# Kernel tuning notes

Measured on AMD Instinct MI355X. Metric: run time of the kernel, lower is better.

The kernel has to match this reference:

```python
import jax, jax.numpy as jnp
import numpy as np

B, T, P = 4, 512, 3584          # batch, new tokens per seq, cached tokens per seq
D_MODEL, H, KH, DH = 2048, 16, 4, 128
N_REP = H // KH
MAX_SEQ = 4096
ROPE_BASE = 1e6
EPS = 1e-6


def _rmsnorm(t, w):
    # t: [..., DH]
    var = jnp.mean(t * t, axis=-1, keepdims=True)
    return t * jax.lax.rsqrt(var + EPS) * w


def _rope(t, positions):
    # t: [N, heads, DH], positions: [N] int
    half = DH // 2
    inv_freq = (1.0 / ROPE_BASE) ** (2.0 * jnp.arange(half, dtype=jnp.float32) / DH)
    theta = positions.astype(jnp.float32)[:, None] * inv_freq[None, :]   # [N, half]
    theta = jnp.concatenate([theta, theta], axis=-1)                      # [N, DH]
    sin = jnp.sin(theta)[:, None, :]
    cos = jnp.cos(theta)[:, None, :]
    x1, x2 = jnp.split(t, 2, axis=-1)
    rot = jnp.concatenate([-x2, x1], axis=-1)
    return cos * t + sin * rot


def setup_inputs() -> dict:
    key = jax.random.key(0)
    ks = jax.random.split(key, 9)
    N = B * T
    x = jax.random.normal(ks[0], (N, D_MODEL), dtype=jnp.float32)
    k_cache = jax.random.normal(ks[1], (B, KH, P, DH), dtype=jnp.float32)
    v_cache = jax.random.normal(ks[2], (B, KH, P, DH), dtype=jnp.float32)
    s = 1.0 / np.sqrt(D_MODEL)
    w_q = jax.random.normal(ks[3], (H * DH, D_MODEL), dtype=jnp.float32) * s
    w_k = jax.random.normal(ks[4], (KH * DH, D_MODEL), dtype=jnp.float32) * s
    w_v = jax.random.normal(ks[5], (KH * DH, D_MODEL), dtype=jnp.float32) * s
    w_o = jax.random.normal(ks[6], (D_MODEL, H * DH), dtype=jnp.float32) * s
    q_norm_w = jnp.ones((DH,), dtype=jnp.float32)
    k_norm_w = jnp.ones((DH,), dtype=jnp.float32)
    # each sequence's new tokens occupy absolute positions [P, P+T)
    positions = jnp.tile(P + jnp.arange(T, dtype=jnp.int32), B)  # [B*T]
    return {"x": x, "k_cache": k_cache, "v_cache": v_cache,
            "w_q": w_q, "w_k": w_k, "w_v": w_v, "w_o": w_o,
            "q_norm_w": q_norm_w, "k_norm_w": k_norm_w,
            "positions": positions}


def reference(x, k_cache, v_cache, w_q, w_k, w_v, w_o, q_norm_w, k_norm_w, positions):
    N = x.shape[0]
    # QKV projections (no bias)
    q = (x @ w_q.T).reshape(N, H, DH)
    k = (x @ w_k.T).reshape(N, KH, DH)
    v = (x @ w_v.T).reshape(N, KH, DH)
    # per-head RMSNorm then RoPE at absolute positions
    q = _rope(_rmsnorm(q, q_norm_w), positions)
    k = _rope(_rmsnorm(k, k_norm_w), positions)
    # assemble full KV: cached (pre-rotated) past + new tokens
    k_new = k.reshape(B, T, KH, DH).transpose(0, 2, 1, 3)   # [B,KH,T,DH]
    v_new = v.reshape(B, T, KH, DH).transpose(0, 2, 1, 3)
    k_full = jnp.concatenate([k_cache, k_new], axis=2)       # [B,KH,P+T,DH]
    v_full = jnp.concatenate([v_cache, v_new], axis=2)
    # GQA: repeat each kv head n_rep times
    k_rep = jnp.repeat(k_full, N_REP, axis=1)                # [B,H,S,DH]
    v_rep = jnp.repeat(v_full, N_REP, axis=1)
    q4 = q.reshape(B, T, H, DH).transpose(0, 2, 1, 3)        # [B,H,T,DH]
    scale = 1.0 / jnp.sqrt(jnp.float32(DH))
    scores = jnp.einsum('bhtd,bhsd->bhts', q4, k_rep) * scale  # [B,H,T,P+T]
    # right-bottom causal mask: q_pos = P + t, kv_pos = s
    q_pos = P + jnp.arange(T)
    kv_pos = jnp.arange(P + T)
    mask = q_pos[:, None] >= kv_pos[None, :]
    scores = jnp.where(mask[None, None], scores, -jnp.inf)
    attn = jax.nn.softmax(scores, axis=-1)
    out = jnp.einsum('bhts,bhsd->bhtd', attn, v_rep)          # [B,H,T,DH]
    out = out.transpose(0, 2, 1, 3).reshape(N, H * DH)
    return out @ w_o.T
```

## Files before the change

### kernel.cpp

```cpp
#include <hip/hip_runtime.h>
#include <hip/hip_bf16.h>
#include <stdint.h>

#define B_   4
#define T_   512
#define P_   3584
#define S_   4096
#define H_   16
#define KH_  4
#define DM_  2048
#define DH_  128
#define NTOK 2048
#define NCHUNK 3
#define NROWS 32768

typedef __attribute__((ext_vector_type(8)))  short          bf16x8;
typedef __attribute__((ext_vector_type(4)))  float          f32x4;
typedef __attribute__((ext_vector_type(16))) float          f32x16;
typedef __attribute__((ext_vector_type(4)))  float          f4v;
typedef __attribute__((ext_vector_type(4)))  unsigned short us4v;

__device__ __forceinline__ unsigned short f2bf(float x) {
    union { float f; unsigned u; } v; v.f = x;
    unsigned r = v.u + 0x7FFFu + ((v.u >> 16) & 1u);
    return (unsigned short)(r >> 16);
}
__device__ __forceinline__ float bf2f(unsigned short b) {
    union { unsigned u; float f; } v; v.u = ((unsigned)b) << 16; return v.f;
}
__device__ __forceinline__ unsigned pkbf(float a, float b) {
    __hip_bfloat162 h = __float22bfloat162_rn(float2{a, b});
    union { __hip_bfloat162 h; unsigned u; } cv; cv.h = h; return cv.u;
}
__device__ __forceinline__ float ex2(float x) {
    float r; asm("v_exp_f32 %0, %1" : "=v"(r) : "v"(x)); return r;
}
__device__ __forceinline__ float max3f(float a, float b, float c) {
    float r; asm("v_max3_f32 %0, %1, %2, %3" : "=v"(r) : "v"(a), "v"(b), "v"(c)); return r;
}
__device__ __forceinline__ float sin_rev(float xf) {
    float r; asm("v_sin_f32 %0, %1" : "=v"(r) : "v"(xf)); return r;
}
__device__ __forceinline__ float cos_rev(float xf) {
    float r; asm("v_cos_f32 %0, %1" : "=v"(r) : "v"(xf)); return r;
}

#define GLDS16(gp, lp) __builtin_amdgcn_global_load_lds( \
    (const __attribute__((address_space(1))) void*)(gp), \
    (__attribute__((address_space(3))) void*)(lp), 16, 0, 0)

__global__ __launch_bounds__(256) void convert_all(
    const float* __restrict__ x,  const float* __restrict__ wq,
    const float* __restrict__ wk, const float* __restrict__ wv,
    const float* __restrict__ wo, const float* __restrict__ kc,
    unsigned short* __restrict__ xb,   unsigned short* __restrict__ wqkvb,
    unsigned short* __restrict__ wob,  unsigned short* __restrict__ kfull)
{
    const long total = 5505024;
    for (long i = (long)blockIdx.x * 256 + threadIdx.x; i < total;
         i += (long)gridDim.x * 256) {
        const f4v* src; us4v* dst; long s4, d4;
        if (i < 1048576)      { src=(const f4v*)x;  dst=(us4v*)xb;              s4=i;         d4=s4; }
        else if (i < 2097152) { src=(const f4v*)wq; dst=(us4v*)wqkvb;           s4=i-1048576; d4=s4; }
        else if (i < 2359296) { src=(const f4v*)wk; dst=(us4v*)(wqkvb+4194304); s4=i-2097152; d4=s4; }
        else if (i < 2621440) { src=(const f4v*)wv; dst=(us4v*)(wqkvb+5242880); s4=i-2359296; d4=s4; }
        else if (i < 3670016) { src=(const f4v*)wo; dst=(us4v*)wob;             s4=i-2621440; d4=s4; }
        else                  { s4=i-3670016; long bk=s4/114688;
                                d4=bk*131072+(s4-bk*114688);
                                src=(const f4v*)kc; dst=(us4v*)kfull; }
        f4v v = src[s4];
        us4v o; o[0]=f2bf(v[0]); o[1]=f2bf(v[1]); o[2]=f2bf(v[2]); o[3]=f2bf(v[3]);
        dst[d4] = o;
    }
}

__global__ __launch_bounds__(256) void vcache_transpose(
    const float* __restrict__ vc, unsigned short* __restrict__ vT)
{
    __shared__ unsigned short tile[64][65];
    const int bk = blockIdx.z;
    const int st = blockIdx.x;
    const int dt = blockIdx.y;
    const float* src = vc + ((size_t)bk * P_ + st * 64) * DH_ + dt * 64;
    const int tq = threadIdx.x & 15;
    const int ts = threadIdx.x >> 4;
    #pragma unroll
    for (int i = 0; i < 4; ++i) {
        const int si = ts + i * 16;
        f4v v = *(const f4v*)(src + (size_t)si * DH_ + tq * 4);
        tile[si][tq*4+0] = f2bf(v[0]); tile[si][tq*4+1] = f2bf(v[1]);
        tile[si][tq*4+2] = f2bf(v[2]); tile[si][tq*4+3] = f2bf(v[3]);
    }
    __syncthreads();
    unsigned short* dst = vT + ((size_t)bk * DH_ + dt * 64) * S_ + st * 64;
    const int sq = threadIdx.x & 15;
    const int td = threadIdx.x >> 4;
    #pragma unroll
    for (int i = 0; i < 4; ++i) {
        const int di = td + i * 16;
        us4v o;
        o[0] = tile[sq*4+0][di]; o[1] = tile[sq*4+1][di];
        o[2] = tile[sq*4+2][di]; o[3] = tile[sq*4+3][di];
        *(us4v*)(dst + (size_t)di * S_ + sq * 4) = o;
    }
}

__global__ __launch_bounds__(256) void gemm_bt(
    const unsigned short* __restrict__ A, const unsigned short* __restrict__ Bw,
    void* __restrict__ C, int M, int N, int K, int obf16)
{
    __shared__ short As[2][128 * 32];
    __shared__ short Bs[2][128 * 32];
    const int tid = threadIdx.x, lane = tid & 63, w = tid >> 6;
    const int nbn = N >> 7;
    const int bm = blockIdx.x / nbn, bn = blockIdx.x % nbn;
    const int m0 = bm << 7, n0 = bn << 7;
    const int wm = w >> 1, wn = w & 1;

    f32x4 acc[4][4];
    #pragma unroll
    for (int i = 0; i < 4; ++i)
        #pragma unroll
        for (int j = 0; j < 4; ++j)
            #pragma unroll
            for (int r = 0; r < 4; ++r) acc[i][j][r] = 0.f;

    const int arow = lane >> 2;
    const int acol = (lane & 3) << 3;

    auto stage = [&](int buf, int k0) {
        #pragma unroll
        for (int cc = 0; cc < 2; ++cc) {
            const int c = 2 * w + cc;
            GLDS16(A  + (size_t)(m0 + c * 16 + arow) * K + k0 + acol, &As[buf][c * 512]);
            GLDS16(Bw + (size_t)(n0 + c * 16 + arow) * K + k0 + acol, &Bs[buf][c * 512]);
        }
    };

    stage(0, 0);
    __syncthreads();

    const int nk = K >> 5;
    const int fr = lane & 15, fk = (lane >> 4) << 3;
    for (int t = 0; t < nk; ++t) {
        const int buf = t & 1;
        if (t + 1 < nk) stage(buf ^ 1, (t + 1) << 5);
        bf16x8 a[4], b[4];
        #pragma unroll
        for (int i = 0; i < 4; ++i)
            a[i] = *(const bf16x8*)&As[buf][(wm * 64 + i * 16 + fr) * 32 + fk];
        #pragma unroll
        for (int j = 0; j < 4; ++j)
            b[j] = *(const bf16x8*)&Bs[buf][(wn * 64 + j * 16 + fr) * 32 + fk];
        #pragma unroll
        for (int i = 0; i < 4; ++i)
            #pragma unroll
            for (int j = 0; j < 4; ++j)
                acc[i][j] = __builtin_amdgcn_mfma_f32_16x16x32_bf16(a[i], b[j], acc[i][j], 0, 0, 0);
        __syncthreads();
    }

    const int er = lane >> 4, ec = lane & 15;
    #pragma unroll
    for (int i = 0; i < 4; ++i)
        #pragma unroll
        for (int j = 0; j < 4; ++j)
            #pragma unroll
            for (int r = 0; r < 4; ++r) {
                const int row = m0 + wm * 64 + i * 16 + er * 4 + r;
                const int col = n0 + wn * 64 + j * 16 + ec;
                if (obf16) ((unsigned short*)C)[(size_t)row * N + col] = f2bf(acc[i][j][r]);
                else       ((float*)C)[(size_t)row * N + col] = acc[i][j][r];
            }
}

__global__ __launch_bounds__(256) void norm_rope(
    const unsigned short* __restrict__ qkv, const float* __restrict__ qw,
    const float* __restrict__ kw,  const int* __restrict__ pos,
    unsigned short* __restrict__ Qb, unsigned short* __restrict__ Kf,
    unsigned short* __restrict__ VT)
{
    const int task = blockIdx.x * 4 + (threadIdx.x >> 6);
    const int n = task / 24, idx = task % 24;
    const int lane = threadIdx.x & 63;
    const int b = n >> 9, t = n & 511;

    if (idx >= 20) {
        const int kh = idx - 20;
        const unsigned short* src = qkv + (size_t)n * 3072 + 2560 + kh * 128;
        unsigned short* dstT = VT + (size_t)(b * KH_ + kh) * DH_ * S_ + (P_ + t);
        dstT[(size_t)lane * S_]        = src[lane];
        dstT[(size_t)(lane + 64) * S_] = src[lane + 64];
        return;
    }
    const bool isq = idx < 16;
    const int hh = isq ? idx : (idx - 16);
    const unsigned short* src = qkv + (size_t)n * 3072 + (isq ? hh * 128 : 2048 + hh * 128);
    const float* wn_ = isq ? qw : kw;
    float x0 = bf2f(src[lane]), x1 = bf2f(src[lane + 64]);
    float ss = x0 * x0 + x1 * x1;
    #pragma unroll
    for (int m = 1; m < 64; m <<= 1) ss += __shfl_xor(ss, m);
    const float rinv = rsqrtf(ss * (1.0f / 128.0f) + 1e-6f);
    float y0 = x0 * rinv * wn_[lane];
    float y1 = x1 * rinv * wn_[lane + 64];
    const float fr = ex2(-(float)lane * (19.931568569324174f / 64.0f));
    const float th = (float)pos[n] * fr;
    const float xr = th * 0.15915494309189535f;
    const float xf = xr - floorf(xr);
    const float sn = sin_rev(xf), cs = cos_rev(xf);
    float o0 = cs * y0 - sn * y1;
    float o1 = cs * y1 + sn * y0;
    unsigned short* dst;
    if (isq) {
        const float qs = 0.08838834764831845f * 1.4426950408889634f;
        o0 *= qs; o1 *= qs;
        dst = Qb + ((size_t)(b * H_ + hh) * T_ + t) * DH_;
    } else {
        dst = Kf + ((size_t)(b * KH_ + hh) * S_ + P_ + t) * DH_;
    }
    dst[lane]      = f2bf(o0);
    dst[lane + 64] = f2bf(o1);
}

__global__ __launch_bounds__(256, 3) void attn(
    const unsigned short* __restrict__ Qb, const unsigned short* __restrict__ Kf,
    const unsigned short* __restrict__ VT, unsigned short* __restrict__ op0,
    unsigned short* __restrict__ op1, unsigned short* __restrict__ op2,
    float2* __restrict__ ml)
{
    __shared__ short Ks[3][32 * 128];
    __shared__ short Vs[3][128 * 32];

    const int tid = threadIdx.x, lane = tid & 63, w = tid >> 6;
    const int c = blockIdx.x >> 8;
    const int y = blockIdx.x & 255;
    const int xcd = y & 7, slot = y >> 3;
    const int p = xcd + 8 * (slot >> 4);
    const int inner = slot & 15;
    const int b = p >> 2, kvh = p & 3;
    const int h = kvh * 4 + (inner >> 2);
    const int qt = inner & 3;
    const int t0 = qt * 128;

    const unsigned short* Qrow = Qb + (size_t)(b * H_ + h) * T_ * DH_;
    const unsigned short* Kb   = Kf + (size_t)(b * KH_ + kvh) * S_ * DH_;
    const unsigned short* VTb  = VT + (size_t)(b * KH_ + kvh) * DH_ * S_;

    const int ql = lane & 31;
    const int hi = lane >> 5;

    bf16x8 qf[8];
    {
        const unsigned short* qp = Qrow + (size_t)(t0 + w * 32 + ql) * DH_ + hi * 8;
        #pragma unroll
        for (int d0 = 0; d0 < 8; ++d0) qf[d0] = *(const bf16x8*)(qp + d0 * 16);
    }

    f32x16 o[4];
    #pragma unroll
    for (int d = 0; d < 4; ++d)
        #pragma unroll
        for (int r = 0; r < 16; ++r) o[d][r] = 0.f;
    float m_run = -INFINITY, l_run = 0.f;

    const int q_pos = P_ + t0 + w * 32 + ql;
    const int s_end_wave = P_ + t0 + w * 32 + 32;
    const int nt_full = (P_ + t0 + 128) >> 5;
    const int nj = (nt_full - c + 2) / 3;

    auto stage = [&](int buf, int tile) {
        const int s0 = tile << 5;
        #pragma unroll
        for (int cc = 0; cc < 2; ++cc) {
            const int cx = 2 * w + cc;
            const int krow = cx * 4 + (lane >> 4);
            const int kel  = 8 * ((lane & 15) ^ (krow & 15));
            GLDS16(Kb + (size_t)(s0 + krow) * DH_ + kel, &Ks[buf][cx * 512]);
            const int vrow = cx * 16 + (lane >> 2);
            const int vel  = 8 * ((lane & 3) ^ ((lane >> 3) & 3));
            GLDS16(VTb + (size_t)vrow * S_ + s0 + vel, &Vs[buf][cx * 512]);
        }
    };

    stage(0, c);
    if (nj > 1) stage(1, c + 3);

    for (int j = 0; j < nj; ++j) {
        if (j + 1 < nj) asm volatile("s_waitcnt vmcnt(4)" ::: "memory");
        else            asm volatile("s_waitcnt vmcnt(0)" ::: "memory");
        __builtin_amdgcn_s_barrier();
        if (j + 2 < nj) stage((j + 2) % 3, c + 3 * (j + 2));

        const int t = c + 3 * j;
        const int s0 = t << 5;
        const int buf = j % 3;
        if (s0 < s_end_wave) {
            f32x16 st;
            #pragma unroll
            for (int r = 0; r < 16; ++r) st[r] = 0.f;
            {
                const char* kbase = (const char*)&Ks[buf][0] + ql * 256;
                const int sw = 16 * (ql & 15);
                #pragma unroll
                for (int d0 = 0; d0 < 8; ++d0) {
                    bf16x8 kfr = *(const bf16x8*)(kbase + ((d0 * 32 + 16 * hi) ^ sw));
                    st = __builtin_amdgcn_mfma_f32_32x32x16_bf16(kfr, qf[d0], st, 0, 0, 0);
                }
            }
            if (s0 + 31 > P_ + t0 + w * 32) {
                #pragma unroll
                for (int r = 0; r < 16; ++r) {
                    const int srow = (r & 3) + 8 * (r >> 2) + 4 * hi;
                    if (s0 + srow > q_pos) st[r] = -INFINITY;
                }
            }
            float m0_ = max3f(st[0], st[1], st[2]),  m1_ = max3f(st[3], st[4], st[5]);
            float m2_ = max3f(st[6], st[7], st[8]),  m3_ = max3f(st[9], st[10], st[11]);
            float m4_ = max3f(st[12], st[13], st[14]);
            float pmax = fmaxf(max3f(m0_, m1_, m2_), max3f(m3_, m4_, st[15]));
            pmax = fmaxf(pmax, __shfl_xor(pmax, 32));
            if (!__all(pmax <= m_run + 11.5f)) {
                const float m_new = fmaxf(m_run, pmax);
                const float alpha = ex2(m_run - m_new);
                l_run *= alpha;
                #pragma unroll
                for (int r = 0; r < 16; ++r) {
                    const int qr = (r & 3) + 8 * (r >> 2) + 4 * hi;
                    const float a = __shfl(alpha, qr);
                    #pragma unroll
                    for (int d = 0; d < 4; ++d) o[d][r] *= a;
                }
                m_run = m_new;
            }
            float pv[16]; float psum = 0.f;
            #pragma unroll
            for (int r = 0; r < 16; ++r) { pv[r] = ex2(st[r] - m_run); psum += pv[r]; }
            psum += __shfl_xor(psum, 32);
            l_run += psum;
            unsigned pk[8];
            #pragma unroll
            for (int u = 0; u < 8; ++u) pk[u] = pkbf(pv[2 * u], pv[2 * u + 1]);
            unsigned xw[8];
            #pragma unroll
            for (int u = 0; u < 8; ++u) xw[u] = (unsigned)__shfl_xor((int)pk[u], 32);
            union { bf16x8 v; unsigned u[4]; } pa0, pa1;
            pa0.u[0] = hi ? xw[2] : pk[0];  pa0.u[1] = hi ? xw[3] : pk[1];
            pa0.u[2] = hi ? pk[2] : xw[0];  pa0.u[3] = hi ? pk[3] : xw[1];
            pa1.u[0] = hi ? xw[6] : pk[4];  pa1.u[1] = hi ? xw[7] : pk[5];
            pa1.u[2] = hi ? pk[6] : xw[4];  pa1.u[3] = hi ? pk[7] : xw[5];
            #pragma unroll
            for (int ch = 0; ch < 2; ++ch)
                #pragma unroll
                for (int db = 0; db < 4; ++db) {
                    const int vrow = db * 32 + ql;
                    bf16x8 vf = *(const bf16x8*)&Vs[buf][vrow * 32 + 8 * ((2 * ch + hi) ^ ((ql >> 1) & 3))];
                    o[db] = __builtin_amdgcn_mfma_f32_32x32x16_bf16(
                        ch ? pa1.v : pa0.v, vf, o[db], 0, 0, 0);
                }
        }
    }

    unsigned short* op = (c == 0) ? op0 : (c == 1) ? op1 : op2;
    const int rowbase = (b * H_ + h) * T_ + t0 + w * 32;
    if (hi == 0) ml[c * NROWS + rowbase + ql] = float2{m_run, l_run};
    #pragma unroll
    for (int r = 0; r < 16; ++r) {
        const int qr = (r & 3) + 8 * (r >> 2) + 4 * hi;
        unsigned short* orow = op + (size_t)(rowbase + qr) * DH_;
        #pragma unroll
        for (int d = 0; d < 4; ++d)
            orow[d * 32 + ql] = f2bf(o[d][r]);
    }
}

__global__ __launch_bounds__(256) void combine(
    const float2* __restrict__ ml,
    const unsigned short* __restrict__ op0, const unsigned short* __restrict__ op1,
    const unsigned short* __restrict__ op2, unsigned short* __restrict__ ao)
{
    const int row = blockIdx.x * 4 + (threadIdx.x >> 6);
    const int lane = threadIdx.x & 63;
    const float2 a0 = ml[row], a1 = ml[NROWS + row], a2 = ml[2 * NROWS + row];
    const float m = fmaxf(a0.x, fmaxf(a1.x, a2.x));
    const float w0 = ex2(a0.x - m), w1 = ex2(a1.x - m), w2 = ex2(a2.x - m);
    const float Linv = 1.0f / (w0 * a0.y + w1 * a1.y + w2 * a2.y);
    const size_t src = (size_t)row * DH_ + 2 * lane;
    const unsigned u0 = *(const unsigned*)(op0 + src);
    const unsigned u1 = *(const unsigned*)(op1 + src);
    const unsigned u2 = *(const unsigned*)(op2 + src);
    const float v0 = (bf2f((unsigned short)u0) * w0 + bf2f((unsigned short)u1) * w1 +
                      bf2f((unsigned short)u2) * w2) * Linv;
    const float v1 = (bf2f((unsigned short)(u0 >> 16)) * w0 + bf2f((unsigned short)(u1 >> 16)) * w1 +
                      bf2f((unsigned short)(u2 >> 16)) * w2) * Linv;
    const int t = row & 511, h = (row >> 9) & 15, b = row >> 13;
    unsigned short* dst = ao + ((size_t)(b * T_ + t) * (H_ * DH_)) + h * DH_ + 2 * lane;
    *(unsigned*)dst = pkbf(v0, v1);
}

extern "C" void kernel_launch(void* const* d_in, const int* in_sizes, int n_in,
                              void* d_out, int out_size, void* d_ws, size_t ws_size,
                              hipStream_t stream)
{
    const float* x   = (const float*)d_in[0];
    const float* kc  = (const float*)d_in[1];
    const float* vc  = (const float*)d_in[2];
    const float* wq  = (const float*)d_in[3];
    const float* wk  = (const float*)d_in[4];
    const float* wv  = (const float*)d_in[5];
    const float* wo  = (const float*)d_in[6];
    const float* qnw = (const float*)d_in[7];
    const float* knw = (const float*)d_in[8];
    const int*   pos = (const int*)d_in[9];
    float* out = (float*)d_out;

    char* ws = (char*)d_ws;
    unsigned short* xb    = (unsigned short*)(ws + 0);
    unsigned short* wqkvb = (unsigned short*)(ws + 8388608);
    unsigned short* wob   = (unsigned short*)(ws + 20971520);
    unsigned short* qkvb  = (unsigned short*)(ws + 29360128);
    unsigned short* qb    = (unsigned short*)(ws + 41943040);
    unsigned short* kfull = (unsigned short*)(ws + 50331648);
    unsigned short* vT    = (unsigned short*)(ws + 67108864);
    unsigned short* ao    = (unsigned short*)(ws + 83886080);
    unsigned short* op0   = (unsigned short*)(ws + 0);
    unsigned short* op1   = (unsigned short*)(ws + 8388608);
    float2*         ml    = (float2*)(ws + 16777216);
    unsigned short* op2   = (unsigned short*)(ws + 29360128);

    hipLaunchKernelGGL(convert_all, dim3(2048), dim3(256), 0, stream,
                       x, wq, wk, wv, wo, kc, xb, wqkvb, wob, kfull);
    hipLaunchKernelGGL(vcache_transpose, dim3(P_ / 64, 2, B_ * KH_), dim3(256), 0, stream,
                       vc, vT);
    hipLaunchKernelGGL(gemm_bt, dim3(16 * 24), dim3(256), 0, stream,
                       xb, wqkvb, (void*)qkvb, 2048, 3072, 2048, 1);
    hipLaunchKernelGGL(norm_rope, dim3(NTOK * 24 / 4), dim3(256), 0, stream,
                       qkvb, qnw, knw, pos, qb, kfull, vT);
    hipLaunchKernelGGL(attn, dim3(NCHUNK * 256), dim3(256), 0, stream,
                       qb, kfull, vT, op0, op1, op2, ml);
    hipLaunchKernelGGL(combine, dim3(NROWS / 4), dim3(256), 0, stream,
                       ml, op0, op1, op2, ao);
    hipLaunchKernelGGL(gemm_bt, dim3(16 * 16), dim3(256), 0, stream,
                       ao, wob, (void*)out, 2048, 2048, 2048, 0);
}
```

Baseline: 229.7 us.

## Fuse V-cache transpose into convert kernel, remap GEMM tiles per XCD, split QK chains

Result: no change. 231.8 us (+0.9%).

```diff
diff --git a/kernel.cpp b/kernel.cpp
--- a/kernel.cpp
+++ b/kernel.cpp
@@ -53,12 +53,45 @@
     const float* __restrict__ x,  const float* __restrict__ wq,
     const float* __restrict__ wk, const float* __restrict__ wv,
     const float* __restrict__ wo, const float* __restrict__ kc,
+    const float* __restrict__ vc,
     unsigned short* __restrict__ xb,   unsigned short* __restrict__ wqkvb,
-    unsigned short* __restrict__ wob,  unsigned short* __restrict__ kfull)
-{
+    unsigned short* __restrict__ wob,  unsigned short* __restrict__ kfull,
+    unsigned short* __restrict__ vT)
+{
+    __shared__ unsigned short tile[64][65];
+    if (blockIdx.x >= 2048) {
+        const int id = blockIdx.x - 2048;
+        const int bk = id / 112;
+        const int rem = id % 112;
+        const int st = rem >> 1;
+        const int dt = rem & 1;
+        const float* src = vc + ((size_t)bk * P_ + st * 64) * DH_ + dt * 64;
+        const int tq = threadIdx.x & 15;
+        const int ts = threadIdx.x >> 4;
+        #pragma unroll
+        for (int i = 0; i < 4; ++i) {
+            const int si = ts + i * 16;
+            f4v v = *(const f4v*)(src + (size_t)si * DH_ + tq * 4);
+            tile[si][tq*4+0] = f2bf(v[0]); tile[si][tq*4+1] = f2bf(v[1]);
+            tile[si][tq*4+2] = f2bf(v[2]); tile[si][tq*4+3] = f2bf(v[3]);
+        }
+        __syncthreads();
+        unsigned short* dst = vT + ((size_t)bk * DH_ + dt * 64) * S_ + st * 64;
+        const int sq = threadIdx.x & 15;
+        const int td = threadIdx.x >> 4;
+        #pragma unroll
+        for (int i = 0; i < 4; ++i) {
+            const int di = td + i * 16;
+            us4v o;
+            o[0] = tile[sq*4+0][di]; o[1] = tile[sq*4+1][di];
+            o[2] = tile[sq*4+2][di]; o[3] = tile[sq*4+3][di];
+            *(us4v*)(dst + (size_t)di * S_ + sq * 4) = o;
+        }
+        return;
+    }
     const long total = 5505024;
     for (long i = (long)blockIdx.x * 256 + threadIdx.x; i < total;
-         i += (long)gridDim.x * 256) {
+         i += 2048L * 256) {
         const f4v* src; us4v* dst; long s4, d4;
         if (i < 1048576)      { src=(const f4v*)x;  dst=(us4v*)xb;              s4=i;         d4=s4; }
         else if (i < 2097152) { src=(const f4v*)wq; dst=(us4v*)wqkvb;           s4=i-1048576; d4=s4; }
@@ -74,37 +107,6 @@
     }
 }
 
-__global__ __launch_bounds__(256) void vcache_transpose(
-    const float* __restrict__ vc, unsigned short* __restrict__ vT)
-{
-    __shared__ unsigned short tile[64][65];
-    const int bk = blockIdx.z;
-    const int st = blockIdx.x;
-    const int dt = blockIdx.y;
-    const float* src = vc + ((size_t)bk * P_ + st * 64) * DH_ + dt * 64;
-    const int tq = threadIdx.x & 15;
-    const int ts = threadIdx.x >> 4;
-    #pragma unroll
-    for (int i = 0; i < 4; ++i) {
-        const int si = ts + i * 16;
-        f4v v = *(const f4v*)(src + (size_t)si * DH_ + tq * 4);
-        tile[si][tq*4+0] = f2bf(v[0]); tile[si][tq*4+1] = f2bf(v[1]);
-        tile[si][tq*4+2] = f2bf(v[2]); tile[si][tq*4+3] = f2bf(v[3]);
-    }
-    __syncthreads();
-    unsigned short* dst = vT + ((size_t)bk * DH_ + dt * 64) * S_ + st * 64;
-    const int sq = threadIdx.x & 15;
-    const int td = threadIdx.x >> 4;
-    #pragma unroll
-    for (int i = 0; i < 4; ++i) {
-        const int di = td + i * 16;
-        us4v o;
-        o[0] = tile[sq*4+0][di]; o[1] = tile[sq*4+1][di];
-        o[2] = tile[sq*4+2][di]; o[3] = tile[sq*4+3][di];
-        *(us4v*)(dst + (size_t)di * S_ + sq * 4) = o;
-    }
-}
-
 __global__ __launch_bounds__(256) void gemm_bt(
     const unsigned short* __restrict__ A, const unsigned short* __restrict__ Bw,
     void* __restrict__ C, int M, int N, int K, int obf16)
@@ -113,7 +115,10 @@
     __shared__ short Bs[2][128 * 32];
     const int tid = threadIdx.x, lane = tid & 63, w = tid >> 6;
     const int nbn = N >> 7;
-    const int bm = blockIdx.x / nbn, bn = blockIdx.x % nbn;
+    const int cpx = nbn >> 3;
+    const int xcd = blockIdx.x & 7;
+    const int rr = blockIdx.x >> 3;
+    const int bm = rr / cpx, bn = xcd * cpx + rr % cpx;
     const int m0 = bm << 7, n0 = bn << 7;
     const int wm = w >> 1, wn = w & 1;
 
@@ -152,11 +157,13 @@
         #pragma unroll
         for (int j = 0; j < 4; ++j)
             b[j] = *(const bf16x8*)&Bs[buf][(wn * 64 + j * 16 + fr) * 32 + fk];
+        __builtin_amdgcn_s_setprio(1);
         #pragma unroll
         for (int i = 0; i < 4; ++i)
             #pragma unroll
             for (int j = 0; j < 4; ++j)
                 acc[i][j] = __builtin_amdgcn_mfma_f32_16x16x32_bf16(a[i], b[j], acc[i][j], 0, 0, 0);
+        __builtin_amdgcn_s_setprio(0);
         __syncthreads();
     }
 
@@ -296,18 +303,25 @@
         const int s0 = t << 5;
         const int buf = j % 3;
         if (s0 < s_end_wave) {
-            f32x16 st;
-            #pragma unroll
-            for (int r = 0; r < 16; ++r) st[r] = 0.f;
+            f32x16 st0, st1;
+            #pragma unroll
+            for (int r = 0; r < 16; ++r) { st0[r] = 0.f; st1[r] = 0.f; }
             {
                 const char* kbase = (const char*)&Ks[buf][0] + ql * 256;
                 const int sw = 16 * (ql & 15);
+                __builtin_amdgcn_s_setprio(1);
                 #pragma unroll
-                for (int d0 = 0; d0 < 8; ++d0) {
-                    bf16x8 kfr = *(const bf16x8*)(kbase + ((d0 * 32 + 16 * hi) ^ sw));
-                    st = __builtin_amdgcn_mfma_f32_32x32x16_bf16(kfr, qf[d0], st, 0, 0, 0);
+                for (int d0 = 0; d0 < 4; ++d0) {
+                    bf16x8 kf0 = *(const bf16x8*)(kbase + ((d0 * 32 + 16 * hi) ^ sw));
+                    bf16x8 kf1 = *(const bf16x8*)(kbase + (((d0 + 4) * 32 + 16 * hi) ^ sw));
+                    st0 = __builtin_amdgcn_mfma_f32_32x32x16_bf16(kf0, qf[d0], st0, 0, 0, 0);
+                    st1 = __builtin_amdgcn_mfma_f32_32x32x16_bf16(kf1, qf[d0 + 4], st1, 0, 0, 0);
                 }
+                __builtin_amdgcn_s_setprio(0);
             }
+            f32x16 st;
+            #pragma unroll
+            for (int r = 0; r < 16; ++r) st[r] = st0[r] + st1[r];
             if (s0 + 31 > P_ + t0 + w * 32) {
                 #pragma unroll
                 for (int r = 0; r < 16; ++r) {
@@ -349,6 +363,7 @@
             pa0.u[2] = hi ? pk[2] : xw[0];  pa0.u[3] = hi ? pk[3] : xw[1];
             pa1.u[0] = hi ? xw[6] : pk[4];  pa1.u[1] = hi ? xw[7] : pk[5];
             pa1.u[2] = hi ? pk[6] : xw[4];  pa1.u[3] = hi ? pk[7] : xw[5];
+            __builtin_amdgcn_s_setprio(1);
             #pragma unroll
             for (int ch = 0; ch < 2; ++ch)
                 #pragma unroll
@@ -358,6 +373,7 @@
                     o[db] = __builtin_amdgcn_mfma_f32_32x32x16_bf16(
                         ch ? pa1.v : pa0.v, vf, o[db], 0, 0, 0);
                 }
+            __builtin_amdgcn_s_setprio(0);
         }
     }
 
@@ -428,10 +444,8 @@
     float2*         ml    = (float2*)(ws + 16777216);
     unsigned short* op2   = (unsigned short*)(ws + 29360128);
 
-    hipLaunchKernelGGL(convert_all, dim3(2048), dim3(256), 0, stream,
-                       x, wq, wk, wv, wo, kc, xb, wqkvb, wob, kfull);
-    hipLaunchKernelGGL(vcache_transpose, dim3(P_ / 64, 2, B_ * KH_), dim3(256), 0, stream,
-                       vc, vT);
+    hipLaunchKernelGGL(convert_all, dim3(2048 + 1792), dim3(256), 0, stream,
+                       x, wq, wk, wv, wo, kc, vc, xb, wqkvb, wob, kfull, vT);
     hipLaunchKernelGGL(gemm_bt, dim3(16 * 24), dim3(256), 0, stream,
                        xb, wqkvb, (void*)qkvb, 2048, 3072, 2048, 1);
     hipLaunchKernelGGL(norm_rope, dim3(NTOK * 24 / 4), dim3(256), 0, stream,
```
